# Kernel optimization log

Measured on AMD Instinct MI355X. Metric: run time of the kernel, lower is better.

## Reference

```python
import math
import jax, jax.numpy as jnp
import numpy as np

B, N, D, H, HID = 2, 2048, 1024, 16, 4096
KS = (7, 25, 49)

def _alibi_slopes(n):
    def p2(m):
        start = 2.0 ** (-(2.0 ** (-(math.log2(m) - 3))))
        return [start * (start ** i) for i in range(m)]
    if math.log2(n).is_integer():
        s = p2(n)
    else:
        cp2 = 2 ** int(math.floor(math.log2(n)))
        s = p2(cp2) + p2(2 * cp2)[0::2][: n - cp2]
    return jnp.asarray(s, dtype=jnp.float32)

def _ln(x, g, b, eps=1e-5):
    m = x.mean(-1, keepdims=True)
    v = ((x - m) ** 2).mean(-1, keepdims=True)
    return (x - m) / jnp.sqrt(v + eps) * g + b

def _dwconv(x, w, pl, pr, mode, bias=None):
    # x: (B, D, L) channels-first, w: (D, 1, k) depthwise kernel
    xp = jnp.pad(x, ((0, 0), (0, 0), (pl, pr)), mode=mode)
    y = jax.lax.conv_general_dilated(xp, w, (1,), 'VALID',
                                     dimension_numbers=('NCH', 'OIH', 'NCH'),
                                     feature_group_count=x.shape[1])
    if bias is not None:
        y = y + bias[None, :, None]
    return y

def _forward(x, periodic_bias, alpha, dw7, dw25, dw49, ln1_g, ln1_b, ln2_g, ln2_b,
             Wq, bq, Wk, bk, Wv, bv, Wo, bo, W1, b1, W2, b2, tw, tb):
    Bx, Nx, Dm = x.shape
    hd = Dm // H
    # --- series decomposition: softmax-weighted multi-scale moving averages ---
    xt = x.transpose(0, 2, 1)  # (B, D, N)
    branches = [_dwconv(xt, w, k // 2, k // 2, 'reflect')
                for w, k in ((dw7, 7), (dw25, 25), (dw49, 49))]
    wmix = jax.nn.softmax(alpha)
    T = sum(br * wi for br, wi in zip(branches, wmix)).transpose(0, 2, 1)  # trend (B,N,D)
    S = x - T  # seasonal
    # --- ALiBi self-attention on normalized seasonal part ---
    sn = _ln(S, ln1_g, ln1_b)
    q = (jnp.einsum('bnd,ed->bne', sn, Wq) + bq).reshape(Bx, Nx, H, hd)
    k = (jnp.einsum('bnd,ed->bne', sn, Wk) + bk).reshape(Bx, Nx, H, hd)
    v = (jnp.einsum('bnd,ed->bne', sn, Wv) + bv).reshape(Bx, Nx, H, hd)
    logits = jnp.einsum('bqhd,bkhd->bhqk', q, k) / np.float32(np.sqrt(hd))
    idx = jnp.arange(Nx)
    dist = jnp.maximum(idx[None, :] - idx[:, None], 0).astype(jnp.float32)  # clamp(j-i, 0)
    slopes = _alibi_slopes(H)
    logits = logits - slopes[None, :, None, None] * dist[None, None] + periodic_bias[None, None]
    attn = jax.nn.softmax(logits, axis=-1)
    o = jnp.einsum('bhqk,bkhd->bqhd', attn, v).reshape(Bx, Nx, Dm)
    y = jnp.einsum('bnd,ed->bne', o, Wo) + bo
    x_s = S + y
    # --- dense FFN (exact GELU, as torch nn.GELU default) ---
    h = _ln(x_s, ln2_g, ln2_b)
    ffn = jnp.einsum('bnh,dh->bnd',
                     jax.nn.gelu(jnp.einsum('bnd,hd->bnh', h, W1) + b1, approximate=False),
                     W2) + b2
    x_s = x_s + ffn
    # --- trend path: depthwise conv k=5, zero padding 2 ---
    t_out = _dwconv(T.transpose(0, 2, 1), tw, 2, 2, 'constant', tb).transpose(0, 2, 1)
    return x_s + t_out

def setup_inputs():
    key = jax.random.key(0)
    ks = jax.random.split(key, 12)
    def lin(k, o, i):
        return jax.random.normal(k, (o, i), jnp.float32) / np.float32(np.sqrt(i))
    return {
        'x': jax.random.normal(ks[0], (B, N, D), jnp.float32),
        'periodic_bias': 0.1 * jax.random.normal(ks[1], (N, N), jnp.float32),
        'alpha': jnp.zeros((len(KS),), jnp.float32),
        'dw7': jnp.full((D, 1, 7), 1.0 / 7, jnp.float32),
        'dw25': jnp.full((D, 1, 25), 1.0 / 25, jnp.float32),
        'dw49': jnp.full((D, 1, 49), 1.0 / 49, jnp.float32),
        'ln1_g': jnp.ones((D,), jnp.float32), 'ln1_b': jnp.zeros((D,), jnp.float32),
        'ln2_g': jnp.ones((D,), jnp.float32), 'ln2_b': jnp.zeros((D,), jnp.float32),
        'Wq': lin(ks[2], D, D), 'bq': jnp.zeros((D,), jnp.float32),
        'Wk': lin(ks[3], D, D), 'bk': jnp.zeros((D,), jnp.float32),
        'Wv': lin(ks[4], D, D), 'bv': jnp.zeros((D,), jnp.float32),
        'Wo': lin(ks[5], D, D), 'bo': jnp.zeros((D,), jnp.float32),
        'W1': lin(ks[6], HID, D), 'b1': jnp.zeros((HID,), jnp.float32),
        'W2': lin(ks[7], D, HID), 'b2': jnp.zeros((D,), jnp.float32),
        'tw': 0.1 * jax.random.normal(ks[8], (D, 1, 5), jnp.float32),
        'tb': jnp.zeros((D,), jnp.float32),
    }

def reference(x, periodic_bias, alpha, dw7, dw25, dw49, ln1_g, ln1_b, ln2_g, ln2_b,
              Wq, bq, Wk, bk, Wv, bv, Wo, bo, W1, b1, W2, b2, tw, tb):
    out = _forward(x, periodic_bias, alpha, dw7, dw25, dw49, ln1_g, ln1_b, ln2_g, ln2_b,
                   Wq, bq, Wk, bk, Wv, bv, Wo, bo, W1, b1, W2, b2, tw, tb)
    return (out, jnp.zeros((), out.dtype))
```

## Files before the change

kernel.cpp:

```cpp
#include <hip/hip_runtime.h>
#include <cstdint>

#define BB 2
#define NN 2048
#define DD 1024
#define HH 16
#define HD 64
#define HID_ 4096
#define MM (BB*NN)

typedef __bf16 bf16x8 __attribute__((ext_vector_type(8)));
typedef float  f32x4  __attribute__((ext_vector_type(4)));

__device__ inline void gload_lds16(const void* g, void* l) {
  __builtin_amdgcn_global_load_lds((const __attribute__((address_space(1))) char*)g,
                                   (__attribute__((address_space(3))) char*)l, 16, 0, 0);
}

__global__ void k_wcomb(const float* __restrict__ alpha, const float* __restrict__ dw7,
                        const float* __restrict__ dw25, const float* __restrict__ dw49,
                        float* __restrict__ wc) {
  int t = blockIdx.x;
  float a0 = alpha[0], a1 = alpha[1], a2 = alpha[2];
  float mx = fmaxf(a0, fmaxf(a1, a2));
  float e0 = __expf(a0 - mx), e1 = __expf(a1 - mx), e2 = __expf(a2 - mx);
  float inv = 1.f / (e0 + e1 + e2);
  float w0 = e0 * inv, w1 = e1 * inv, w2 = e2 * inv;
  for (int d = threadIdx.x; d < DD; d += blockDim.x) {
    float v = w2 * dw49[d * 49 + t];
    if (t >= 12 && t <= 36) v += w1 * dw25[d * 25 + (t - 12)];
    if (t >= 21 && t <= 27) v += w0 * dw7[d * 7 + (t - 21)];
    wc[t * DD + d] = v;
  }
}

__global__ void k_bias3(const float* __restrict__ bq, const float* __restrict__ bk,
                        const float* __restrict__ bv, float* __restrict__ b3) {
  for (int i = threadIdx.x; i < 3 * DD; i += blockDim.x) {
    const float* s = (i < DD) ? bq : (i < 2 * DD ? bk : bv);
    b3[i] = s[i & (DD - 1)];
  }
}

__global__ __launch_bounds__(256) void k_cvtall(const float* __restrict__ Wq, const float* __restrict__ Wk,
                         const float* __restrict__ Wv, const float* __restrict__ Wo,
                         const float* __restrict__ W1, const float* __restrict__ W2,
                         __bf16* __restrict__ dst) {
  size_t i = ((size_t)blockIdx.x * 256 + threadIdx.x) * 4;
  const float* s;
  if (i < 1048576u) s = Wq + i;
  else if (i < 2097152u) s = Wk + (i - 1048576u);
  else if (i < 3145728u) s = Wv + (i - 2097152u);
  else if (i < 4194304u) s = Wo + (i - 3145728u);
  else if (i < 8388608u) s = W1 + (i - 4194304u);
  else s = W2 + (i - 8388608u);
  float4 v = *(const float4*)s;
  dst[i] = (__bf16)v.x; dst[i+1] = (__bf16)v.y; dst[i+2] = (__bf16)v.z; dst[i+3] = (__bf16)v.w;
}

__global__ __launch_bounds__(256) void k_pbt(const float* __restrict__ pb,
                                             __bf16* __restrict__ pbt) {
  int q = blockIdx.x;
  int qt16 = q >> 4, qm = q & 15;
  for (int k = threadIdx.x; k < NN; k += 256) {
    float v = pb[(size_t)q * NN + k] * 1.4426950408889634f;
    int kt = k >> 4, g = (k >> 2) & 3, rr = k & 3;
    pbt[((size_t)qt16 * 128 + kt) * 256 + (qm + 16 * g) * 4 + rr] = (__bf16)v;
  }
}

__global__ __launch_bounds__(256) void k_decomp(const float* __restrict__ x,
                                                const float* __restrict__ wc,
                                                float* __restrict__ T, float* __restrict__ S) {
  int bid = blockIdx.x;
  int db = bid & 3, ns = (bid >> 2) & 127, b = bid >> 9;
  int d = db * 256 + threadIdx.x;
  const float* xb = x + (size_t)b * NN * DD + d;
  float xw[64];
#pragma unroll
  for (int i = 0; i < 64; ++i) {
    int n = ns * 16 - 24 + i;
    n = (n < 0) ? -n : n;
    n = (n > NN - 1) ? 2 * (NN - 1) - n : n;
    xw[i] = xb[(size_t)n * DD];
  }
  float acc[16];
#pragma unroll
  for (int i = 0; i < 16; ++i) acc[i] = 0.f;
#pragma unroll
  for (int t = 0; t < 49; ++t) {
    float wv = wc[t * DD + d];
#pragma unroll
    for (int i = 0; i < 16; ++i) acc[i] = fmaf(wv, xw[i + t], acc[i]);
  }
  size_t base = ((size_t)b * NN + ns * 16) * DD + d;
#pragma unroll
  for (int i = 0; i < 16; ++i) {
    T[base + (size_t)i * DD] = acc[i];
    S[base + (size_t)i * DD] = xw[i + 24] - acc[i];
  }
}

__global__ __launch_bounds__(256) void k_tout(const float* __restrict__ T,
                                              const float* __restrict__ tw,
                                              const float* __restrict__ tb,
                                              float* __restrict__ tout) {
  int bid = blockIdx.x;
  int db = bid & 3, ns = (bid >> 2) & 127, b = bid >> 9;
  int d = db * 256 + threadIdx.x;
  const float* Tb = T + (size_t)b * NN * DD + d;
  float xw[20];
#pragma unroll
  for (int i = 0; i < 20; ++i) {
    int n = ns * 16 - 2 + i;
    xw[i] = (n < 0 || n >= NN) ? 0.f : Tb[(size_t)n * DD];
  }
  float bv = tb[d];
  float acc[16];
#pragma unroll
  for (int i = 0; i < 16; ++i) acc[i] = bv;
#pragma unroll
  for (int t = 0; t < 5; ++t) {
    float wv = tw[d * 5 + t];
#pragma unroll
    for (int i = 0; i < 16; ++i) acc[i] = fmaf(wv, xw[i + t], acc[i]);
  }
  size_t base = ((size_t)b * NN + ns * 16) * DD + d;
#pragma unroll
  for (int i = 0; i < 16; ++i) tout[base + (size_t)i * DD] = acc[i];
}

__global__ __launch_bounds__(256) void k_ln(const float* __restrict__ x,
                                            const float* __restrict__ g,
                                            const float* __restrict__ bt,
                                            __bf16* __restrict__ y) {
  int row = blockIdx.x;
  const float* xr = x + (size_t)row * DD;
  int i = threadIdx.x * 4;
  float4 v = *(const float4*)&xr[i];
  float s = v.x + v.y + v.z + v.w;
  float sq = v.x * v.x + v.y * v.y + v.z * v.z + v.w * v.w;
#pragma unroll
  for (int m = 1; m <= 32; m <<= 1) { s += __shfl_xor(s, m); sq += __shfl_xor(sq, m); }
  __shared__ float rs[4], rq[4];
  int wid = threadIdx.x >> 6;
  if ((threadIdx.x & 63) == 0) { rs[wid] = s; rq[wid] = sq; }
  __syncthreads();
  s = rs[0] + rs[1] + rs[2] + rs[3];
  sq = rq[0] + rq[1] + rq[2] + rq[3];
  float mean = s * (1.f / DD);
  float var = sq * (1.f / DD) - mean * mean;
  float rstd = rsqrtf(var + 1e-5f);
  float4 gv = *(const float4*)&g[i];
  float4 bv = *(const float4*)&bt[i];
  __bf16* yr = y + (size_t)row * DD + i;
  yr[0] = (__bf16)((v.x - mean) * rstd * gv.x + bv.x);
  yr[1] = (__bf16)((v.y - mean) * rstd * gv.y + bv.y);
  yr[2] = (__bf16)((v.z - mean) * rstd * gv.z + bv.z);
  yr[3] = (__bf16)((v.w - mean) * rstd * gv.w + bv.w);
}

template <int EPI, int BNT>
__global__ __launch_bounds__(256) void k_gemm(const __bf16* __restrict__ A,
                                              const __bf16* __restrict__ Bw, int K,
                                              const float* __restrict__ bias,
                                              const float* __restrict__ aux1,
                                              const float* __restrict__ aux2,
                                              float* __restrict__ outf,
                                              __bf16* __restrict__ outb) {
  constexpr int NFR = BNT / 32;
  __shared__ __bf16 aS[2][128 * 32];
  __shared__ __bf16 bS[2][BNT * 32];
  const int tid = threadIdx.x;
  const int lane = tid & 63;
  const int wid = tid >> 6;
  const int wm = wid >> 1, wn = wid & 1;
  const int r = lane & 15, gq = lane >> 4;
  const int m0 = blockIdx.y * 128;
  const int n0 = blockIdx.x * BNT;

  f32x4 acc[4][NFR];
#pragma unroll
  for (int mi = 0; mi < 4; ++mi)
#pragma unroll
    for (int ni = 0; ni < NFR; ++ni) acc[mi][ni] = (f32x4){0.f, 0.f, 0.f, 0.f};

  auto stage = [&](int bufi, int k0) {
#pragma unroll
    for (int i = 0; i < 2; ++i) {
      int e = i * 2048 + tid * 8;
      int row = e >> 5, col = e & 31;
      gload_lds16(A + (size_t)(m0 + row) * K + k0 + col, &aS[bufi][e]);
    }
#pragma unroll
    for (int i = 0; i < BNT / 64; ++i) {
      int e = i * 2048 + tid * 8;
      int row = e >> 5, col = e & 31;
      gload_lds16(Bw + (size_t)(n0 + row) * K + k0 + col, &bS[bufi][e]);
    }
  };

  stage(0, 0);
  const int nk = K >> 5;
  int buf = 0;
  for (int kt = 0; kt < nk; ++kt) {
    __syncthreads();
    if (kt + 1 < nk) stage(buf ^ 1, (kt + 1) << 5);
    bf16x8 af[4], bfr[NFR];
#pragma unroll
    for (int mi = 0; mi < 4; ++mi)
      af[mi] = *reinterpret_cast<const bf16x8*>(&aS[buf][(wm * 64 + mi * 16 + r) * 32 + gq * 8]);
#pragma unroll
    for (int ni = 0; ni < NFR; ++ni)
      bfr[ni] = *reinterpret_cast<const bf16x8*>(&bS[buf][(wn * (BNT / 2) + ni * 16 + r) * 32 + gq * 8]);
#pragma unroll
    for (int mi = 0; mi < 4; ++mi)
#pragma unroll
      for (int ni = 0; ni < NFR; ++ni)
        acc[mi][ni] = __builtin_amdgcn_mfma_f32_16x16x32_bf16(af[mi], bfr[ni], acc[mi][ni], 0, 0, 0);
    buf ^= 1;
  }

#pragma unroll
  for (int mi = 0; mi < 4; ++mi) {
#pragma unroll
    for (int ni = 0; ni < NFR; ++ni) {
      int colg = n0 + wn * (BNT / 2) + ni * 16 + r;
      float bcol = bias[colg];
#pragma unroll
      for (int rr = 0; rr < 4; ++rr) {
        int mg = m0 + wm * 64 + mi * 16 + gq * 4 + rr;
        float val = acc[mi][ni][rr] + bcol;
        if constexpr (EPI == 0) {
          int which = colg >> 10, e = colg & 1023;
          int hh = e >> 6, d = e & 63;
          int b = mg >> 11, nq = mg & (NN - 1);
          if (which == 2) {
            int nl = nq & 63, kk = nl & 31;
            int slot = ((kk >> 4) << 2) | (((kk >> 2) & 3) << 3) | (kk & 3) | (nl & 32);
            int nqp = (nq & ~63) | slot;
            outb[(size_t)2 * (BB * HH * NN * HD) +
                 ((size_t)((b * HH + hh) * HD + d)) * NN + nqp] = (__bf16)val;
          } else {
            outb[(size_t)which * (BB * HH * NN * HD) +
                 ((size_t)(b * HH + hh) * NN + nq) * HD + d] = (__bf16)val;
          }
        } else if constexpr (EPI == 1) {
          size_t idx = (size_t)mg * DD + colg;
          outf[idx] = aux1[idx] + val;
        } else if constexpr (EPI == 2) {
          float gl = val * 0.5f * (1.f + erff(val * 0.70710678118f));
          outb[(size_t)mg * HID_ + colg] = (__bf16)gl;
        } else {
          size_t idx = (size_t)mg * DD + colg;
          outf[idx] = val + aux1[idx] + aux2[idx];
        }
      }
    }
  }
}

__global__ __launch_bounds__(512) void k_attn(const __bf16* __restrict__ qb,
                                              const __bf16* __restrict__ kb,
                                              const __bf16* __restrict__ vtb,
                                              const __bf16* __restrict__ pbt,
                                              __bf16* __restrict__ ob) {
  __shared__ __bf16 kS[2][64 * 64];
  __shared__ __bf16 vS[2][64 * 64];
  int blk = blockIdx.x;
  int qt = blk & 15, bh = blk >> 4;
  int h = bh & (HH - 1), b = bh >> 4;
  int tid = threadIdx.x;
  int lane = tid & 63, w = tid >> 6;
  int r = lane & 15, g = lane >> 4;
  const __bf16* Kp = kb + (size_t)bh * NN * HD;
  const __bf16* Vt = vtb + (size_t)bh * HD * NN;
  int qbase = qt * 128 + w * 16;
  int cq = qt * 2 + (w >> 2);
  const __bf16* Q = qb + ((size_t)bh * NN + qbase) * HD;

  bf16x8 qf0 = *(const bf16x8*)&Q[(size_t)r * HD + g * 8];
  bf16x8 qf1 = *(const bf16x8*)&Q[(size_t)r * HD + 32 + g * 8];
  bf16x8 onesf;
#pragma unroll
  for (int j = 0; j < 8; ++j) onesf[j] = (__bf16)1.0f;

  const float C = 0.18033688011112042f;
  const float THRL2 = 11.541560327111707f;
  float slope = exp2f(-0.5f * (float)(h + 1)) * 1.4426950408889634f;
  float sconst[16];
#pragma unroll
  for (int st = 0; st < 4; ++st)
#pragma unroll
    for (int rr = 0; rr < 4; ++rr) sconst[st * 4 + rr] = slope * (float)(st * 16 + rr);
  float aL = slope * (float)(g * 4 - r);

  float m = 0.f;
  f32x4 oacc[4], lacc;
#pragma unroll
  for (int t = 0; t < 4; ++t) oacc[t] = (f32x4){0.f, 0.f, 0.f, 0.f};
  lacc = (f32x4){0.f, 0.f, 0.f, 0.f};

  auto stage = [&](int bufi, int kc0) {
    int row = tid >> 3;
    int c = (tid & 7) * 8;
    int src = c ^ ((row & 7) * 8);
    gload_lds16(Kp + (size_t)(kc0 + row) * HD + src, &kS[bufi][tid * 8]);
    gload_lds16(Vt + (size_t)row * NN + kc0 + src, &vS[bufi][tid * 8]);
  };

  stage(0, 0);
  int buf = 0;
  size_t tilebase = (size_t)(qt * 8 + w) * 128;
  int sw = (r & 7) * 8;

  for (int ch = 0; ch < NN / 64; ++ch) {
    int kc0 = ch * 64;
    __syncthreads();
    if (ch + 1 < NN / 64) stage(buf ^ 1, kc0 + 64);

    uint2 ub[4];
#pragma unroll
    for (int st = 0; st < 4; ++st)
      ub[st] = *(const uint2*)&pbt[(tilebase + (kc0 >> 4) + st) * 256 + lane * 4];

    f32x4 sacc[4];
#pragma unroll
    for (int st = 0; st < 4; ++st) {
      sacc[st] = (f32x4){0.f, 0.f, 0.f, 0.f};
      int rowb = (st * 16 + r) * 64;
      bf16x8 kf0 = *(const bf16x8*)&kS[buf][rowb + ((g * 8) ^ sw)];
      bf16x8 kf1 = *(const bf16x8*)&kS[buf][rowb + ((32 + g * 8) ^ sw)];
      sacc[st] = __builtin_amdgcn_mfma_f32_16x16x32_bf16(kf0, qf0, sacc[st], 0, 0, 0);
      sacc[st] = __builtin_amdgcn_mfma_f32_16x16x32_bf16(kf1, qf1, sacc[st], 0, 0, 0);
    }

    float zm[16];
    if (ch > cq) {
      float uu = fmaf(slope, (float)(kc0 - qbase), aL) + m;
#pragma unroll
      for (int st = 0; st < 4; ++st) {
        float p0 = __uint_as_float(ub[st].x << 16);
        float p1 = __uint_as_float(ub[st].x & 0xffff0000u);
        float p2 = __uint_as_float(ub[st].y << 16);
        float p3 = __uint_as_float(ub[st].y & 0xffff0000u);
        zm[st*4+0] = fmaf(sacc[st][0], C, p0) - uu - sconst[st*4+0];
        zm[st*4+1] = fmaf(sacc[st][1], C, p1) - uu - sconst[st*4+1];
        zm[st*4+2] = fmaf(sacc[st][2], C, p2) - uu - sconst[st*4+2];
        zm[st*4+3] = fmaf(sacc[st][3], C, p3) - uu - sconst[st*4+3];
      }
    } else if (ch < cq) {
#pragma unroll
      for (int st = 0; st < 4; ++st) {
        float p0 = __uint_as_float(ub[st].x << 16);
        float p1 = __uint_as_float(ub[st].x & 0xffff0000u);
        float p2 = __uint_as_float(ub[st].y << 16);
        float p3 = __uint_as_float(ub[st].y & 0xffff0000u);
        zm[st*4+0] = fmaf(sacc[st][0], C, p0) - m;
        zm[st*4+1] = fmaf(sacc[st][1], C, p1) - m;
        zm[st*4+2] = fmaf(sacc[st][2], C, p2) - m;
        zm[st*4+3] = fmaf(sacc[st][3], C, p3) - m;
      }
    } else {
      int kqb = kc0 + g * 4 - qbase - r;
#pragma unroll
      for (int st = 0; st < 4; ++st) {
        float p0 = __uint_as_float(ub[st].x << 16);
        float p1 = __uint_as_float(ub[st].x & 0xffff0000u);
        float p2 = __uint_as_float(ub[st].y << 16);
        float p3 = __uint_as_float(ub[st].y & 0xffff0000u);
        float pb4[4] = {p0, p1, p2, p3};
#pragma unroll
        for (int rr = 0; rr < 4; ++rr) {
          int dk = kqb + st * 16 + rr;
          float dist = (dk > 0) ? (float)dk : 0.f;
          zm[st*4+rr] = fmaf(sacc[st][rr], C, pb4[rr]) - fmaf(slope, dist, m);
        }
      }
    }

    float zmax = zm[0];
#pragma unroll
    for (int j = 1; j < 16; ++j) zmax = fmaxf(zmax, zm[j]);
    if (__any(zmax > THRL2)) {
      float rowmax = fmaxf(zmax, __shfl_xor(zmax, 16));
      rowmax = fmaxf(rowmax, __shfl_xor(rowmax, 32));
      float delta = fmaxf(rowmax, 0.f);
      m += delta;
      float sc = exp2f(-delta);
      float sco[4];
#pragma unroll
      for (int rr = 0; rr < 4; ++rr) sco[rr] = __shfl(sc, g * 4 + rr);
#pragma unroll
      for (int rr = 0; rr < 4; ++rr) {
        lacc[rr] *= sco[rr];
#pragma unroll
        for (int t = 0; t < 4; ++t) oacc[t][rr] *= sco[rr];
      }
#pragma unroll
      for (int j = 0; j < 16; ++j) zm[j] -= delta;
    }

    bf16x8 pa0, pa1;
#pragma unroll
    for (int j = 0; j < 8; ++j) {
      pa0[j] = (__bf16)exp2f(zm[(j >> 2) * 4 + (j & 3)]);
      pa1[j] = (__bf16)exp2f(zm[(2 + (j >> 2)) * 4 + (j & 3)]);
    }

#pragma unroll
    for (int t = 0; t < 4; ++t) {
      int rowb = (t * 16 + r) * 64;
      bf16x8 vf0 = *(const bf16x8*)&vS[buf][rowb + ((g * 8) ^ sw)];
      bf16x8 vf1 = *(const bf16x8*)&vS[buf][rowb + ((32 + g * 8) ^ sw)];
      oacc[t] = __builtin_amdgcn_mfma_f32_16x16x32_bf16(pa0, vf0, oacc[t], 0, 0, 0);
      oacc[t] = __builtin_amdgcn_mfma_f32_16x16x32_bf16(pa1, vf1, oacc[t], 0, 0, 0);
    }
    lacc = __builtin_amdgcn_mfma_f32_16x16x32_bf16(pa0, onesf, lacc, 0, 0, 0);
    lacc = __builtin_amdgcn_mfma_f32_16x16x32_bf16(pa1, onesf, lacc, 0, 0, 0);
    buf ^= 1;
  }

#pragma unroll
  for (int rr = 0; rr < 4; ++rr) {
    int qg = qbase + g * 4 + rr;
    float inv = 1.f / lacc[rr];
#pragma unroll
    for (int t = 0; t < 4; ++t) {
      float v = oacc[t][rr] * inv;
      ob[((size_t)(b * NN) + qg) * DD + h * HD + t * 16 + r] = (__bf16)v;
    }
  }
}

__global__ void k_tail(float* __restrict__ out) { out[(size_t)BB * NN * DD] = 0.f; }

extern "C" void kernel_launch(void* const* d_in, const int* in_sizes, int n_in,
                              void* d_out, int out_size, void* d_ws, size_t ws_size,
                              hipStream_t stream) {
  const float* x    = (const float*)d_in[0];
  const float* pb   = (const float*)d_in[1];
  const float* alpha= (const float*)d_in[2];
  const float* dw7  = (const float*)d_in[3];
  const float* dw25 = (const float*)d_in[4];
  const float* dw49 = (const float*)d_in[5];
  const float* ln1g = (const float*)d_in[6];
  const float* ln1b = (const float*)d_in[7];
  const float* ln2g = (const float*)d_in[8];
  const float* ln2b = (const float*)d_in[9];
  const float* Wq   = (const float*)d_in[10];
  const float* bq   = (const float*)d_in[11];
  const float* Wk   = (const float*)d_in[12];
  const float* bk   = (const float*)d_in[13];
  const float* Wv   = (const float*)d_in[14];
  const float* bv   = (const float*)d_in[15];
  const float* Wo   = (const float*)d_in[16];
  const float* bo   = (const float*)d_in[17];
  const float* W1   = (const float*)d_in[18];
  const float* b1   = (const float*)d_in[19];
  const float* W2   = (const float*)d_in[20];
  const float* b2   = (const float*)d_in[21];
  const float* tw   = (const float*)d_in[22];
  const float* tb   = (const float*)d_in[23];
  float* out = (float*)d_out;

  char* w = (char*)d_ws;
  size_t off = 0;
  auto alloc = [&](size_t bytes) -> char* {
    char* p = w + off;
    off = (off + bytes + 255) & ~(size_t)255;
    return p;
  };
  float*  wc    = (float*)alloc(49 * 1024 * 4);
  float*  b3    = (float*)alloc(3072 * 4);
  float*  Tbuf  = (float*)alloc((size_t)MM * DD * 4);
  float*  Sbuf  = (float*)alloc((size_t)MM * DD * 4);
  float*  toutb = (float*)alloc((size_t)MM * DD * 4);
  __bf16* sn    = (__bf16*)alloc((size_t)MM * DD * 2);
  __bf16* qkv   = (__bf16*)alloc((size_t)3 * MM * DD * 2);
  __bf16* gb    = (__bf16*)alloc((size_t)MM * HID_ * 2);
  __bf16* wall  = (__bf16*)alloc((size_t)12582912 * 2);
  __bf16* pbt   = (__bf16*)alloc((size_t)NN * NN * 2);
  __bf16* wqkvb = wall;
  __bf16* wob   = wall + (size_t)3 * DD * DD;
  __bf16* w1b   = wall + (size_t)4 * DD * DD;
  __bf16* w2b   = wall + (size_t)4 * DD * DD + (size_t)HID_ * DD;
  float*  xs    = Tbuf;
  __bf16* obuf  = sn;
  __bf16* hb    = qkv;

  const size_t BHND = (size_t)BB * HH * NN * HD;

  k_wcomb<<<49, 256, 0, stream>>>(alpha, dw7, dw25, dw49, wc);
  k_bias3<<<1, 256, 0, stream>>>(bq, bk, bv, b3);
  k_pbt<<<NN, 256, 0, stream>>>(pb, pbt);
  k_cvtall<<<12288, 256, 0, stream>>>(Wq, Wk, Wv, Wo, W1, W2, wall);
  k_decomp<<<1024, 256, 0, stream>>>(x, wc, Tbuf, Sbuf);
  k_tout<<<1024, 256, 0, stream>>>(Tbuf, tw, tb, toutb);
  k_ln<<<MM, 256, 0, stream>>>(Sbuf, ln1g, ln1b, sn);
  k_gemm<0,128><<<dim3(24, 32), 256, 0, stream>>>(sn, wqkvb, DD, b3, nullptr, nullptr, nullptr, qkv);
  k_attn<<<BB * HH * (NN / 128), 512, 0, stream>>>(qkv, qkv + BHND, qkv + 2 * BHND, pbt, obuf);
  k_gemm<1,64><<<dim3(16, 32), 256, 0, stream>>>(obuf, wob, DD, bo, Sbuf, nullptr, xs, nullptr);
  k_ln<<<MM, 256, 0, stream>>>(xs, ln2g, ln2b, hb);
  k_gemm<2,128><<<dim3(32, 32), 256, 0, stream>>>(hb, w1b, DD, b1, nullptr, nullptr, nullptr, gb);
  k_gemm<3,64><<<dim3(16, 32), 256, 0, stream>>>(gb, w2b, HID_, b2, xs, toutb, out, nullptr);
  k_tail<<<1, 1, 0, stream>>>(out);
}
```

Baseline: 353.6 us.

## Deepen GEMM K-tile with LDS swizzle, double attention KV chunk, fp32 bias table

```diff
diff --git a/kernel.cpp b/kernel.cpp
--- a/kernel.cpp
+++ b/kernel.cpp
@@ -59,13 +59,13 @@
 }
 
 __global__ __launch_bounds__(256) void k_pbt(const float* __restrict__ pb,
-                                             __bf16* __restrict__ pbt) {
+                                             float* __restrict__ pbt) {
   int q = blockIdx.x;
   int qt16 = q >> 4, qm = q & 15;
   for (int k = threadIdx.x; k < NN; k += 256) {
     float v = pb[(size_t)q * NN + k] * 1.4426950408889634f;
     int kt = k >> 4, g = (k >> 2) & 3, rr = k & 3;
-    pbt[((size_t)qt16 * 128 + kt) * 256 + (qm + 16 * g) * 4 + rr] = (__bf16)v;
+    pbt[((size_t)qt16 * 128 + kt) * 256 + (qm + 16 * g) * 4 + rr] = v;
   }
 }
 
@@ -160,7 +160,7 @@
   yr[3] = (__bf16)((v.w - mean) * rstd * gv.w + bv.w);
 }
 
-template <int EPI, int BNT>
+template <int EPI, int BNT, int BKT>
 __global__ __launch_bounds__(256) void k_gemm(const __bf16* __restrict__ A,
                                               const __bf16* __restrict__ Bw, int K,
                                               const float* __restrict__ bias,
@@ -169,8 +169,9 @@
                                               float* __restrict__ outf,
                                               __bf16* __restrict__ outb) {
   constexpr int NFR = BNT / 32;
-  __shared__ __bf16 aS[2][128 * 32];
-  __shared__ __bf16 bS[2][BNT * 32];
+  constexpr int NKK = BKT / 32;
+  __shared__ __bf16 aS[2][128 * BKT];
+  __shared__ __bf16 bS[2][BNT * BKT];
   const int tid = threadIdx.x;
   const int lane = tid & 63;
   const int wid = tid >> 6;
@@ -178,6 +179,7 @@
   const int r = lane & 15, gq = lane >> 4;
   const int m0 = blockIdx.y * 128;
   const int n0 = blockIdx.x * BNT;
+  const int rsw = (BKT == 64) ? (r & 7) * 8 : 0;
 
   f32x4 acc[4][NFR];
 #pragma unroll
@@ -187,37 +189,47 @@
 
   auto stage = [&](int bufi, int k0) {
 #pragma unroll
-    for (int i = 0; i < 2; ++i) {
+    for (int i = 0; i < (128 * BKT) / 2048; ++i) {
       int e = i * 2048 + tid * 8;
-      int row = e >> 5, col = e & 31;
-      gload_lds16(A + (size_t)(m0 + row) * K + k0 + col, &aS[bufi][e]);
-    }
-#pragma unroll
-    for (int i = 0; i < BNT / 64; ++i) {
+      int row = e / BKT, col = e % BKT;
+      int src = (BKT == 64) ? (col ^ ((row & 7) * 8)) : col;
+      gload_lds16(A + (size_t)(m0 + row) * K + k0 + src, &aS[bufi][e]);
+    }
+#pragma unroll
+    for (int i = 0; i < (BNT * BKT) / 2048; ++i) {
       int e = i * 2048 + tid * 8;
-      int row = e >> 5, col = e & 31;
-      gload_lds16(Bw + (size_t)(n0 + row) * K + k0 + col, &bS[bufi][e]);
+      int row = e / BKT, col = e % BKT;
+      int src = (BKT == 64) ? (col ^ ((row & 7) * 8)) : col;
+      gload_lds16(Bw + (size_t)(n0 + row) * K + k0 + src, &bS[bufi][e]);
     }
   };
 
   stage(0, 0);
-  const int nk = K >> 5;
+  const int nk = K / BKT;
   int buf = 0;
   for (int kt = 0; kt < nk; ++kt) {
     __syncthreads();
-    if (kt + 1 < nk) stage(buf ^ 1, (kt + 1) << 5);
-    bf16x8 af[4], bfr[NFR];
+    if (kt + 1 < nk) stage(buf ^ 1, (kt + 1) * BKT);
+    bf16x8 af[4][NKK], bfr[NFR][NKK];
 #pragma unroll
     for (int mi = 0; mi < 4; ++mi)
-      af[mi] = *reinterpret_cast<const bf16x8*>(&aS[buf][(wm * 64 + mi * 16 + r) * 32 + gq * 8]);
+#pragma unroll
+      for (int kk = 0; kk < NKK; ++kk)
+        af[mi][kk] = *reinterpret_cast<const bf16x8*>(
+            &aS[buf][(wm * 64 + mi * 16 + r) * BKT + ((kk * 32 + gq * 8) ^ rsw)]);
 #pragma unroll
     for (int ni = 0; ni < NFR; ++ni)
-      bfr[ni] = *reinterpret_cast<const bf16x8*>(&bS[buf][(wn * (BNT / 2) + ni * 16 + r) * 32 + gq * 8]);
-#pragma unroll
-    for (int mi = 0; mi < 4; ++mi)
-#pragma unroll
-      for (int ni = 0; ni < NFR; ++ni)
-        acc[mi][ni] = __builtin_amdgcn_mfma_f32_16x16x32_bf16(af[mi], bfr[ni], acc[mi][ni], 0, 0, 0);
+#pragma unroll
+      for (int kk = 0; kk < NKK; ++kk)
+        bfr[ni][kk] = *reinterpret_cast<const bf16x8*>(
+            &bS[buf][(wn * (BNT / 2) + ni * 16 + r) * BKT + ((kk * 32 + gq * 8) ^ rsw)]);
+#pragma unroll
+    for (int kk = 0; kk < NKK; ++kk)
+#pragma unroll
+      for (int mi = 0; mi < 4; ++mi)
+#pragma unroll
+        for (int ni = 0; ni < NFR; ++ni)
+          acc[mi][ni] = __builtin_amdgcn_mfma_f32_16x16x32_bf16(af[mi][kk], bfr[ni][kk], acc[mi][ni], 0, 0, 0);
     buf ^= 1;
   }
 
@@ -263,10 +275,10 @@
 __global__ __launch_bounds__(512) void k_attn(const __bf16* __restrict__ qb,
                                               const __bf16* __restrict__ kb,
                                               const __bf16* __restrict__ vtb,
-                                              const __bf16* __restrict__ pbt,
+                                              const float* __restrict__ pbt,
                                               __bf16* __restrict__ ob) {
-  __shared__ __bf16 kS[2][64 * 64];
-  __shared__ __bf16 vS[2][64 * 64];
+  __shared__ __bf16 kS[2][128 * 64];
+  __shared__ __bf16 vS[2][64 * 128];
   int blk = blockIdx.x;
   int qt = blk & 15, bh = blk >> 4;
   int h = bh & (HH - 1), b = bh >> 4;
@@ -302,122 +314,124 @@
   lacc = (f32x4){0.f, 0.f, 0.f, 0.f};
 
   auto stage = [&](int bufi, int kc0) {
-    int row = tid >> 3;
-    int c = (tid & 7) * 8;
-    int src = c ^ ((row & 7) * 8);
-    gload_lds16(Kp + (size_t)(kc0 + row) * HD + src, &kS[bufi][tid * 8]);
-    gload_lds16(Vt + (size_t)row * NN + kc0 + src, &vS[bufi][tid * 8]);
+#pragma unroll
+    for (int i = 0; i < 2; ++i) {
+      int idx = i * 512 + tid;
+      int row = idx >> 3, c = (idx & 7) * 8;
+      int src = c ^ ((row & 7) * 8);
+      gload_lds16(Kp + (size_t)(kc0 + row) * HD + src, &kS[bufi][idx * 8]);
+    }
+#pragma unroll
+    for (int i = 0; i < 2; ++i) {
+      int idx = i * 512 + tid;
+      int row = idx >> 4, c = (idx & 15) * 8;
+      int src = (c & 64) | ((c & 63) ^ ((row & 7) * 8));
+      gload_lds16(Vt + (size_t)row * NN + kc0 + src, &vS[bufi][idx * 8]);
+    }
   };
 
   stage(0, 0);
   int buf = 0;
-  size_t tilebase = (size_t)(qt * 8 + w) * 128;
+  const float* pbp = pbt + (size_t)(qt * 8 + w) * 128 * 256 + lane * 4;
   int sw = (r & 7) * 8;
 
-  for (int ch = 0; ch < NN / 64; ++ch) {
-    int kc0 = ch * 64;
+  for (int ch2 = 0; ch2 < NN / 128; ++ch2) {
     __syncthreads();
-    if (ch + 1 < NN / 64) stage(buf ^ 1, kc0 + 64);
-
-    uint2 ub[4];
-#pragma unroll
-    for (int st = 0; st < 4; ++st)
-      ub[st] = *(const uint2*)&pbt[(tilebase + (kc0 >> 4) + st) * 256 + lane * 4];
-
-    f32x4 sacc[4];
-#pragma unroll
-    for (int st = 0; st < 4; ++st) {
-      sacc[st] = (f32x4){0.f, 0.f, 0.f, 0.f};
-      int rowb = (st * 16 + r) * 64;
-      bf16x8 kf0 = *(const bf16x8*)&kS[buf][rowb + ((g * 8) ^ sw)];
-      bf16x8 kf1 = *(const bf16x8*)&kS[buf][rowb + ((32 + g * 8) ^ sw)];
-      sacc[st] = __builtin_amdgcn_mfma_f32_16x16x32_bf16(kf0, qf0, sacc[st], 0, 0, 0);
-      sacc[st] = __builtin_amdgcn_mfma_f32_16x16x32_bf16(kf1, qf1, sacc[st], 0, 0, 0);
-    }
-
-    float zm[16];
-    if (ch > cq) {
-      float uu = fmaf(slope, (float)(kc0 - qbase), aL) + m;
+    if (ch2 + 1 < NN / 128) stage(buf ^ 1, (ch2 + 1) * 128);
+
+#pragma unroll
+    for (int sub = 0; sub < 2; ++sub) {
+      int ch = ch2 * 2 + sub;
+      int kc0 = ch * 64;
+
+      float4 ub[4];
+#pragma unroll
+      for (int st = 0; st < 4; ++st)
+        ub[st] = *(const float4*)(pbp + (size_t)(ch * 4 + st) * 256);
+
+      f32x4 sacc[4];
 #pragma unroll
       for (int st = 0; st < 4; ++st) {
-        float p0 = __uint_as_float(ub[st].x << 16);
-        float p1 = __uint_as_float(ub[st].x & 0xffff0000u);
-        float p2 = __uint_as_float(ub[st].y << 16);
-        float p3 = __uint_as_float(ub[st].y & 0xffff0000u);
-        zm[st*4+0] = fmaf(sacc[st][0], C, p0) - uu - sconst[st*4+0];
-        zm[st*4+1] = fmaf(sacc[st][1], C, p1) - uu - sconst[st*4+1];
-        zm[st*4+2] = fmaf(sacc[st][2], C, p2) - uu - sconst[st*4+2];
-        zm[st*4+3] = fmaf(sacc[st][3], C, p3) - uu - sconst[st*4+3];
+        sacc[st] = (f32x4){0.f, 0.f, 0.f, 0.f};
+        int rowb = (sub * 64 + st * 16 + r) * 64;
+        bf16x8 kf0 = *(const bf16x8*)&kS[buf][rowb + ((g * 8) ^ sw)];
+        bf16x8 kf1 = *(const bf16x8*)&kS[buf][rowb + ((32 + g * 8) ^ sw)];
+        sacc[st] = __builtin_amdgcn_mfma_f32_16x16x32_bf16(kf0, qf0, sacc[st], 0, 0, 0);
+        sacc[st] = __builtin_amdgcn_mfma_f32_16x16x32_bf16(kf1, qf1, sacc[st], 0, 0, 0);
       }
-    } else if (ch < cq) {
-#pragma unroll
-      for (int st = 0; st < 4; ++st) {
-        float p0 = __uint_as_float(ub[st].x << 16);
-        float p1 = __uint_as_float(ub[st].x & 0xffff0000u);
-        float p2 = __uint_as_float(ub[st].y << 16);
-        float p3 = __uint_as_float(ub[st].y & 0xffff0000u);
-        zm[st*4+0] = fmaf(sacc[st][0], C, p0) - m;
-        zm[st*4+1] = fmaf(sacc[st][1], C, p1) - m;
-        zm[st*4+2] = fmaf(sacc[st][2], C, p2) - m;
-        zm[st*4+3] = fmaf(sacc[st][3], C, p3) - m;
-      }
-    } else {
-      int kqb = kc0 + g * 4 - qbase - r;
-#pragma unroll
-      for (int st = 0; st < 4; ++st) {
-        float p0 = __uint_as_float(ub[st].x << 16);
-        float p1 = __uint_as_float(ub[st].x & 0xffff0000u);
-        float p2 = __uint_as_float(ub[st].y << 16);
-        float p3 = __uint_as_float(ub[st].y & 0xffff0000u);
-        float pb4[4] = {p0, p1, p2, p3};
-#pragma unroll
-        for (int rr = 0; rr < 4; ++rr) {
-          int dk = kqb + st * 16 + rr;
-          float dist = (dk > 0) ? (float)dk : 0.f;
-          zm[st*4+rr] = fmaf(sacc[st][rr], C, pb4[rr]) - fmaf(slope, dist, m);
+
+      float zm[16];
+      if (ch > cq) {
+        float uu = fmaf(slope, (float)(kc0 - qbase), aL) + m;
+#pragma unroll
+        for (int st = 0; st < 4; ++st) {
+          zm[st*4+0] = fmaf(sacc[st][0], C, ub[st].x) - uu - sconst[st*4+0];
+          zm[st*4+1] = fmaf(sacc[st][1], C, ub[st].y) - uu - sconst[st*4+1];
+          zm[st*4+2] = fmaf(sacc[st][2], C, ub[st].z) - uu - sconst[st*4+2];
+          zm[st*4+3] = fmaf(sacc[st][3], C, ub[st].w) - uu - sconst[st*4+3];
+        }
+      } else if (ch < cq) {
+#pragma unroll
+        for (int st = 0; st < 4; ++st) {
+          zm[st*4+0] = fmaf(sacc[st][0], C, ub[st].x) - m;
+          zm[st*4+1] = fmaf(sacc[st][1], C, ub[st].y) - m;
+          zm[st*4+2] = fmaf(sacc[st][2], C, ub[st].z) - m;
+          zm[st*4+3] = fmaf(sacc[st][3], C, ub[st].w) - m;
+        }
+      } else {
+        int kqb = kc0 + g * 4 - qbase - r;
+#pragma unroll
+        for (int st = 0; st < 4; ++st) {
+          float pb4[4] = {ub[st].x, ub[st].y, ub[st].z, ub[st].w};
+#pragma unroll
+          for (int rr = 0; rr < 4; ++rr) {
+            int dk = kqb + st * 16 + rr;
+            float dist = (dk > 0) ? (float)dk : 0.f;
+            zm[st*4+rr] = fmaf(sacc[st][rr], C, pb4[rr]) - fmaf(slope, dist, m);
+          }
         }
       }
-    }
-
-    float zmax = zm[0];
-#pragma unroll
-    for (int j = 1; j < 16; ++j) zmax = fmaxf(zmax, zm[j]);
-    if (__any(zmax > THRL2)) {
-      float rowmax = fmaxf(zmax, __shfl_xor(zmax, 16));
-      rowmax = fmaxf(rowmax, __shfl_xor(rowmax, 32));
-      float delta = fmaxf(rowmax, 0.f);
-      m += delta;
-      float sc = exp2f(-delta);
-      float sco[4];
-#pragma unroll
-      for (int rr = 0; rr < 4; ++rr) sco[rr] = __shfl(sc, g * 4 + rr);
-#pragma unroll
-      for (int rr = 0; rr < 4; ++rr) {
-        lacc[rr] *= sco[rr];
-#pragma unroll
-        for (int t = 0; t < 4; ++t) oacc[t][rr] *= sco[rr];
+
+      float zmax = zm[0];
+#pragma unroll
+      for (int j = 1; j < 16; ++j) zmax = fmaxf(zmax, zm[j]);
+      if (__any(zmax > THRL2)) {
+        float rowmax = fmaxf(zmax, __shfl_xor(zmax, 16));
+        rowmax = fmaxf(rowmax, __shfl_xor(rowmax, 32));
+        float delta = fmaxf(rowmax, 0.f);
+        m += delta;
+        float sc = exp2f(-delta);
+        float sco[4];
+#pragma unroll
+        for (int rr = 0; rr < 4; ++rr) sco[rr] = __shfl(sc, g * 4 + rr);
+#pragma unroll
+        for (int rr = 0; rr < 4; ++rr) {
+          lacc[rr] *= sco[rr];
+#pragma unroll
+          for (int t = 0; t < 4; ++t) oacc[t][rr] *= sco[rr];
+        }
+#pragma unroll
+        for (int j = 0; j < 16; ++j) zm[j] -= delta;
       }
-#pragma unroll
-      for (int j = 0; j < 16; ++j) zm[j] -= delta;
-    }
-
-    bf16x8 pa0, pa1;
-#pragma unroll
-    for (int j = 0; j < 8; ++j) {
-      pa0[j] = (__bf16)exp2f(zm[(j >> 2) * 4 + (j & 3)]);
-      pa1[j] = (__bf16)exp2f(zm[(2 + (j >> 2)) * 4 + (j & 3)]);
-    }
-
-#pragma unroll
-    for (int t = 0; t < 4; ++t) {
-      int rowb = (t * 16 + r) * 64;
-      bf16x8 vf0 = *(const bf16x8*)&vS[buf][rowb + ((g * 8) ^ sw)];
-      bf16x8 vf1 = *(const bf16x8*)&vS[buf][rowb + ((32 + g * 8) ^ sw)];
-      oacc[t] = __builtin_amdgcn_mfma_f32_16x16x32_bf16(pa0, vf0, oacc[t], 0, 0, 0);
-      oacc[t] = __builtin_amdgcn_mfma_f32_16x16x32_bf16(pa1, vf1, oacc[t], 0, 0, 0);
-    }
-    lacc = __builtin_amdgcn_mfma_f32_16x16x32_bf16(pa0, onesf, lacc, 0, 0, 0);
-    lacc = __builtin_amdgcn_mfma_f32_16x16x32_bf16(pa1, onesf, lacc, 0, 0, 0);
+
+      bf16x8 pa0, pa1;
+#pragma unroll
+      for (int j = 0; j < 8; ++j) {
+        pa0[j] = (__bf16)exp2f(zm[(j >> 2) * 4 + (j & 3)]);
+        pa1[j] = (__bf16)exp2f(zm[(2 + (j >> 2)) * 4 + (j & 3)]);
+      }
+
+#pragma unroll
+      for (int t = 0; t < 4; ++t) {
+        int rowb = (t * 16 + r) * 128 + sub * 64;
+        bf16x8 vf0 = *(const bf16x8*)&vS[buf][rowb + ((g * 8) ^ sw)];
+        bf16x8 vf1 = *(const bf16x8*)&vS[buf][rowb + ((32 + g * 8) ^ sw)];
+        oacc[t] = __builtin_amdgcn_mfma_f32_16x16x32_bf16(pa0, vf0, oacc[t], 0, 0, 0);
+        oacc[t] = __builtin_amdgcn_mfma_f32_16x16x32_bf16(pa1, vf1, oacc[t], 0, 0, 0);
+      }
+      lacc = __builtin_amdgcn_mfma_f32_16x16x32_bf16(pa0, onesf, lacc, 0, 0, 0);
+      lacc = __builtin_amdgcn_mfma_f32_16x16x32_bf16(pa1, onesf, lacc, 0, 0, 0);
+    }
     buf ^= 1;
   }
 
@@ -480,7 +494,7 @@
   __bf16* qkv   = (__bf16*)alloc((size_t)3 * MM * DD * 2);
   __bf16* gb    = (__bf16*)alloc((size_t)MM * HID_ * 2);
   __bf16* wall  = (__bf16*)alloc((size_t)12582912 * 2);
-  __bf16* pbt   = (__bf16*)alloc((size_t)NN * NN * 2);
+  float*  pbt   = (float*)alloc((size_t)NN * NN * 4);
   __bf16* wqkvb = wall;
   __bf16* wob   = wall + (size_t)3 * DD * DD;
   __bf16* w1b   = wall + (size_t)4 * DD * DD;
@@ -498,11 +512,11 @@
   k_decomp<<<1024, 256, 0, stream>>>(x, wc, Tbuf, Sbuf);
   k_tout<<<1024, 256, 0, stream>>>(Tbuf, tw, tb, toutb);
   k_ln<<<MM, 256, 0, stream>>>(Sbuf, ln1g, ln1b, sn);
-  k_gemm<0,128><<<dim3(24, 32), 256, 0, stream>>>(sn, wqkvb, DD, b3, nullptr, nullptr, nullptr, qkv);
+  k_gemm<0,128,32><<<dim3(24, 32), 256, 0, stream>>>(sn, wqkvb, DD, b3, nullptr, nullptr, nullptr, qkv);
   k_attn<<<BB * HH * (NN / 128), 512, 0, stream>>>(qkv, qkv + BHND, qkv + 2 * BHND, pbt, obuf);
-  k_gemm<1,64><<<dim3(16, 32), 256, 0, stream>>>(obuf, wob, DD, bo, Sbuf, nullptr, xs, nullptr);
+  k_gemm<1,64,64><<<dim3(16, 32), 256, 0, stream>>>(obuf, wob, DD, bo, Sbuf, nullptr, xs, nullptr);
   k_ln<<<MM, 256, 0, stream>>>(xs, ln2g, ln2b, hb);
-  k_gemm<2,128><<<dim3(32, 32), 256, 0, stream>>>(hb, w1b, DD, b1, nullptr, nullptr, nullptr, gb);
-  k_gemm<3,64><<<dim3(16, 32), 256, 0, stream>>>(gb, w2b, HID_, b2, xs, toutb, out, nullptr);
+  k_gemm<2,128,32><<<dim3(32, 32), 256, 0, stream>>>(hb, w1b, DD, b1, nullptr, nullptr, nullptr, gb);
+  k_gemm<3,64,64><<<dim3(16, 32), 256, 0, stream>>>(gb, w2b, HID_, b2, xs, toutb, out, nullptr);
   k_tail<<<1, 1, 0, stream>>>(out);
 }
```

Measured after the change: 361.4 us. 2.2% more time.
